# Kernel tuning notes

Measured on AMD Instinct MI355X. Metric: run time of the kernel, lower is better.

Reference implementation:

```python
import jax, jax.numpy as jnp
import numpy as np

USER_NUM = 80000
ITEM_NUM = 40000
N = USER_NUM + ITEM_NUM
EMB = 64
NNZ = 1200000
N_LAYERS = 3


def setup_inputs() -> dict:
    key = jax.random.key(0)
    k1, k2, k3, k4, k5 = jax.random.split(key, 5)
    # xavier_uniform bound for [num, emb]
    bu = float(np.sqrt(6.0 / (USER_NUM + EMB)))
    bi = float(np.sqrt(6.0 / (ITEM_NUM + EMB)))
    user_emb = jax.random.uniform(k1, (USER_NUM, EMB), jnp.float32, -bu, bu)
    item_emb = jax.random.uniform(k2, (ITEM_NUM, EMB), jnp.float32, -bi, bi)
    adj_rows = jax.random.randint(k3, (NNZ,), 0, N, dtype=jnp.int32)
    adj_cols = jax.random.randint(k4, (NNZ,), 0, N, dtype=jnp.int32)
    # normalized-adjacency-like positive values
    adj_vals = jax.random.uniform(k5, (NNZ,), jnp.float32) * (1.0 / 32.0)
    return {"user_emb": user_emb, "item_emb": item_emb,
            "adj_vals": adj_vals, "adj_rows": adj_rows, "adj_cols": adj_cols}


def _spmm(vals, rows, cols, x):
    # out[r] = sum_{e: rows[e]==r} vals[e] * x[cols[e]]   (COO SpMM)
    return jax.ops.segment_sum(vals[:, None] * x[cols], rows, num_segments=N)


def reference(user_emb, item_emb, adj_vals, adj_rows, adj_cols):
    ego = jnp.concatenate([user_emb, item_emb], axis=0)  # [N, d]
    acc = jnp.zeros_like(ego)
    for _ in range(N_LAYERS):
        ego = _spmm(adj_vals, adj_rows, adj_cols, ego)
        acc = acc + ego
    all_emb = acc / N_LAYERS  # mean over stacked layer outputs
    user_all = all_emb[:USER_NUM]
    item_all = all_emb[USER_NUM:]
    return (user_all, item_all)
```

## Files before the change

kernel.cpp:

```cpp
#include <hip/hip_runtime.h>
#include <hip/hip_fp16.h>

#define USER_NUM 80000
#define ITEM_NUM 40000
#define NNODE (USER_NUM + ITEM_NUM)
#define EMB 64
#define NB 469
#define P1_CHUNK 4096

#define HSCALE 8192.0f
#define HINV   (1.0f / 8192.0f)

__global__ void bucket_hist_kernel(const int* __restrict__ rows, int* __restrict__ bcounts, int nnz) {
    __shared__ int h[NB];
    for (int i = threadIdx.x; i < NB; i += blockDim.x) h[i] = 0;
    __syncthreads();
    int nq = nnz >> 2;
    int stride = gridDim.x * blockDim.x;
    for (int i = blockIdx.x * blockDim.x + threadIdx.x; i < nq; i += stride) {
        int4 r = ((const int4*)rows)[i];
        atomicAdd(&h[r.x >> 8], 1);
        atomicAdd(&h[r.y >> 8], 1);
        atomicAdd(&h[r.z >> 8], 1);
        atomicAdd(&h[r.w >> 8], 1);
    }
    if (blockIdx.x == 0) {
        for (int i = (nq << 2) + threadIdx.x; i < nnz; i += blockDim.x)
            atomicAdd(&h[rows[i] >> 8], 1);
    }
    __syncthreads();
    for (int i = threadIdx.x; i < NB; i += blockDim.x)
        if (h[i]) atomicAdd(&bcounts[i], h[i]);
}

__global__ void bucket_scan_kernel(const int* __restrict__ bcounts, int* __restrict__ bucket_off,
                                   int* __restrict__ bcursor, int* __restrict__ row_ptr, int nnz) {
    __shared__ int lds[512];
    int t = threadIdx.x;
    int v = (t < NB) ? bcounts[t] : 0;
    lds[t] = v;
    __syncthreads();
    for (int off = 1; off < 512; off <<= 1) {
        int add = (t >= off) ? lds[t - off] : 0;
        __syncthreads();
        lds[t] += add;
        __syncthreads();
    }
    if (t < NB) {
        int ex = lds[t] - v;
        bucket_off[t] = ex;
        bcursor[t]    = ex;
    }
    if (t == 0) { bucket_off[NB] = nnz; row_ptr[NNODE] = nnz; }
}

__global__ void phase1_kernel(const int* __restrict__ rows, const int* __restrict__ cols,
                              const float* __restrict__ vals, int* __restrict__ bcursor,
                              int2* __restrict__ tmp, int nnz) {
    __shared__ int h[NB];
    __shared__ int base[NB];
    int t = threadIdx.x;
    for (int i = t; i < NB; i += 256) h[i] = 0;
    __syncthreads();
    int lo = blockIdx.x * P1_CHUNK;
    int hi = lo + P1_CHUNK; if (hi > nnz) hi = nnz;
    int n4 = (hi - lo) >> 2;
    const int4*   rows4 = (const int4*)(rows + lo);
    const int4*   cols4 = (const int4*)(cols + lo);
    const float4* vals4 = (const float4*)(vals + lo);

    for (int i = t; i < n4; i += 256) {
        int4 r = rows4[i];
        atomicAdd(&h[r.x >> 8], 1);
        atomicAdd(&h[r.y >> 8], 1);
        atomicAdd(&h[r.z >> 8], 1);
        atomicAdd(&h[r.w >> 8], 1);
    }
    for (int i = lo + (n4 << 2) + t; i < hi; i += 256)
        atomicAdd(&h[rows[i] >> 8], 1);
    __syncthreads();
    for (int i = t; i < NB; i += 256) {
        int c = h[i];
        base[i] = c ? atomicAdd(&bcursor[i], c) : 0;
        h[i] = 0;
    }
    __syncthreads();
    for (int i = t; i < n4; i += 256) {
        int4 r = rows4[i];
        int4 c = cols4[i];
        float4 v = vals4[i];
        {
            int b = r.x >> 8; int loc = atomicAdd(&h[b], 1);
            tmp[base[b] + loc] = make_int2(c.x | ((r.x & 255) << 17), __float_as_int(v.x));
        }
        {
            int b = r.y >> 8; int loc = atomicAdd(&h[b], 1);
            tmp[base[b] + loc] = make_int2(c.y | ((r.y & 255) << 17), __float_as_int(v.y));
        }
        {
            int b = r.z >> 8; int loc = atomicAdd(&h[b], 1);
            tmp[base[b] + loc] = make_int2(c.z | ((r.z & 255) << 17), __float_as_int(v.z));
        }
        {
            int b = r.w >> 8; int loc = atomicAdd(&h[b], 1);
            tmp[base[b] + loc] = make_int2(c.w | ((r.w & 255) << 17), __float_as_int(v.w));
        }
    }
    for (int i = lo + (n4 << 2) + t; i < hi; i += 256) {
        int r = rows[i];
        int b = r >> 8;
        int loc = atomicAdd(&h[b], 1);
        tmp[base[b] + loc] = make_int2(cols[i] | ((r & 255) << 17), __float_as_int(vals[i]));
    }
}

__global__ void phase2_kernel(const int2* __restrict__ tmp, const int* __restrict__ bucket_off,
                              int* __restrict__ row_ptr, int2* __restrict__ edges) {
    __shared__ int hist[256];
    __shared__ int scan[256];
    __shared__ int cur[256];
    int b = blockIdx.x;
    int t = threadIdx.x;
    int row0  = b << 8;
    int nrows = NNODE - row0; if (nrows > 256) nrows = 256;
    int start = bucket_off[b];
    int end   = bucket_off[b + 1];
    hist[t] = 0;
    __syncthreads();
    for (int j = start + t; j < end; j += 256)
        atomicAdd(&hist[tmp[j].x >> 17], 1);
    __syncthreads();
    int v = hist[t];
    scan[t] = v;
    __syncthreads();
    for (int off = 1; off < 256; off <<= 1) {
        int add = (t >= off) ? scan[t - off] : 0;
        __syncthreads();
        scan[t] += add;
        __syncthreads();
    }
    int ex = scan[t] - v + start;
    if (t < nrows) row_ptr[row0 + t] = ex;
    cur[t] = ex;
    __syncthreads();
    for (int j = start + t; j < end; j += 256) {
        int2 e  = tmp[j];
        int rl  = e.x >> 17;
        int pos = atomicAdd(&cur[rl], 1);
        edges[pos] = make_int2(e.x & 0x1FFFF, e.y);
    }
}

__device__ __forceinline__ void load8(long long ev[8], const int2* __restrict__ edges,
                                      int sg, int eg, int j) {
    #pragma unroll
    for (int u = 0; u < 8; ++u) {
        int i = sg + j + u;
        ev[u] = (i < eg) ? *(const long long*)(edges + i) : 0LL;
    }
}

__device__ __forceinline__ float4 unpack_half4(uint2 gv) {
    float2 a = __half22float2(*(const __half2*)&gv.x);
    float2 b = __half22float2(*(const __half2*)&gv.y);
    return make_float4(a.x, a.y, b.x, b.y);
}

template <int LAYER>
__launch_bounds__(256)
__global__ void spmm_kernel(const float* __restrict__ xu, const float* __restrict__ xi,
                            const ushort* __restrict__ xh,
                            const int* __restrict__ row_ptr, const int2* __restrict__ edges,
                            ushort* __restrict__ yh, float* __restrict__ out) {
    int wave = (blockIdx.x * blockDim.x + threadIdx.x) >> 6;
    int lane = threadIdx.x & 63;
    int r0 = wave << 2;
    if (r0 >= NNODE) return;
    int g = lane >> 4;
    int c = lane & 15;

    int rp = 0;
    if (lane < 5) rp = row_ptr[r0 + lane];
    int p0 = __builtin_amdgcn_readlane(rp, 0);
    int p1 = __builtin_amdgcn_readlane(rp, 1);
    int p2 = __builtin_amdgcn_readlane(rp, 2);
    int p3 = __builtin_amdgcn_readlane(rp, 3);
    int p4 = __builtin_amdgcn_readlane(rp, 4);

    int sg = (g == 0) ? p0 : (g == 1) ? p1 : (g == 2) ? p2 : p3;
    int eg = (g == 0) ? p1 : (g == 1) ? p2 : (g == 2) ? p3 : p4;
    int maxd = max(max(p1 - p0, p2 - p1), max(p3 - p2, p4 - p3));

    float4 acc = make_float4(0.f, 0.f, 0.f, 0.f);

    if (maxd > 0) {
        long long ev[8];
        load8(ev, edges, sg, eg, 0);
        for (int j = 0; j < maxd; j += 8) {
            long long evn[8];
            if (j + 8 < maxd) load8(evn, edges, sg, eg, j + 8);
            #pragma unroll
            for (int u = 0; u < 8; ++u) {
                int   col = (int)(unsigned)ev[u];
                float v   = __int_as_float((int)(ev[u] >> 32));
                if (LAYER == 1) {
                    const float* q = (col < USER_NUM) ? xu + (size_t)col * EMB
                                                      : xi + (size_t)(col - USER_NUM) * EMB;
                    float4 gv = ((const float4*)q)[c];
                    acc.x += v * gv.x; acc.y += v * gv.y;
                    acc.z += v * gv.z; acc.w += v * gv.w;
                } else {
                    uint2 hv = ((const uint2*)(xh + (size_t)col * EMB))[c];
                    float4 gv = unpack_half4(hv);
                    acc.x += v * gv.x; acc.y += v * gv.y;
                    acc.z += v * gv.z; acc.w += v * gv.w;
                }
            }
            #pragma unroll
            for (int u = 0; u < 8; ++u) ev[u] = evn[u];
        }
    }

    int row = r0 + g;
    size_t oh = (size_t)row * EMB + (size_t)c * 4;

    if (LAYER == 1) {
        __half2 h0 = __floats2half2_rn(acc.x * HSCALE, acc.y * HSCALE);
        __half2 h1 = __floats2half2_rn(acc.z * HSCALE, acc.w * HSCALE);
        uint2 pk = make_uint2(*(const unsigned*)&h0, *(const unsigned*)&h1);
        *(uint2*)(yh + oh) = pk;
        *(float4*)(out + oh) = acc;
    } else if (LAYER == 2) {
        __half2 h0 = __floats2half2_rn(acc.x, acc.y);
        __half2 h1 = __floats2half2_rn(acc.z, acc.w);
        uint2 pk = make_uint2(*(const unsigned*)&h0, *(const unsigned*)&h1);
        *(uint2*)(yh + oh) = pk;
    } else {
        uint2 own = *(const uint2*)(xh + oh);
        float4 y2v = unpack_half4(own);
        float4 t = *(const float4*)(out + oh);
        const float s = 1.0f / 3.0f;
        t.x = (t.x + (y2v.x + acc.x) * HINV) * s;
        t.y = (t.y + (y2v.y + acc.y) * HINV) * s;
        t.z = (t.z + (y2v.z + acc.z) * HINV) * s;
        t.w = (t.w + (y2v.w + acc.w) * HINV) * s;
        *(float4*)(out + oh) = t;
    }
}

__global__ void init_kernel(const float* __restrict__ user_emb, const float* __restrict__ item_emb,
                            float* __restrict__ x, float* __restrict__ out) {
    int idx = blockIdx.x * blockDim.x + threadIdx.x;
    const int total = NNODE * EMB / 4;
    if (idx >= total) return;
    const int user_total = USER_NUM * EMB / 4;
    float4 v = (idx < user_total) ? ((const float4*)user_emb)[idx]
                                  : ((const float4*)item_emb)[idx - user_total];
    ((float4*)x)[idx]   = v;
    ((float4*)out)[idx] = make_float4(0.f, 0.f, 0.f, 0.f);
}

__global__ void scatter_kernel(const float* __restrict__ x, float* __restrict__ y,
                               const float* __restrict__ vals, const int* __restrict__ rows,
                               const int* __restrict__ cols, int nnz) {
    int tid = blockIdx.x * blockDim.x + threadIdx.x;
    int e = tid >> 4;
    if (e >= nnz) return;
    int c = tid & 15;
    int r = rows[e], col = cols[e];
    float v = vals[e];
    float4 xv = ((const float4*)(x + (size_t)col * EMB))[c];
    float* dst = y + (size_t)r * EMB + (size_t)c * 4;
    atomicAdd(dst + 0, xv.x * v);
    atomicAdd(dst + 1, xv.y * v);
    atomicAdd(dst + 2, xv.z * v);
    atomicAdd(dst + 3, xv.w * v);
}

__global__ void accum_kernel(float* __restrict__ out, const float* __restrict__ y, float scale) {
    int idx = blockIdx.x * blockDim.x + threadIdx.x;
    const int total = NNODE * EMB / 4;
    if (idx >= total) return;
    float4 o = ((float4*)out)[idx];
    float4 a = ((const float4*)y)[idx];
    o.x = (o.x + a.x) * scale; o.y = (o.y + a.y) * scale;
    o.z = (o.z + a.z) * scale; o.w = (o.w + a.w) * scale;
    ((float4*)out)[idx] = o;
}

extern "C" void kernel_launch(void* const* d_in, const int* in_sizes, int n_in,
                              void* d_out, int out_size, void* d_ws, size_t ws_size,
                              hipStream_t stream) {
    const float* user_emb = (const float*)d_in[0];
    const float* item_emb = (const float*)d_in[1];
    const float* vals     = (const float*)d_in[2];
    const int*   rows     = (const int*)d_in[3];
    const int*   cols     = (const int*)d_in[4];
    const int    nnz      = in_sizes[2];

    float* out = (float*)d_out;

    const size_t embN   = (size_t)NNODE * EMB;
    const size_t rp_pad = 120064;

    size_t need = (2 * embN + rp_pad) * 4 + (size_t)nnz * 8;

    if (ws_size >= need) {
        float* bufA    = (float*)d_ws;
        float* bufB    = bufA + embN;
        int*   row_ptr = (int*)(bufB + embN);
        int2*  edges   = (int2*)(row_ptr + rp_pad);

        int2* tmp        = (int2*)bufA;
        int*  bcounts    = (int*)bufB;
        int*  bucket_off = bcounts + 512;
        int*  bcursor    = bucket_off + 512;

        ushort* y1h = (ushort*)bufA;
        ushort* y2h = y1h + embN;

        hipMemsetAsync(bcounts, 0, NB * sizeof(int), stream);
        bucket_hist_kernel<<<256, 256, 0, stream>>>(rows, bcounts, nnz);
        bucket_scan_kernel<<<1, 512, 0, stream>>>(bcounts, bucket_off, bcursor, row_ptr, nnz);
        phase1_kernel<<<(nnz + P1_CHUNK - 1) / P1_CHUNK, 256, 0, stream>>>(rows, cols, vals, bcursor, tmp, nnz);
        phase2_kernel<<<NB, 256, 0, stream>>>(tmp, bucket_off, row_ptr, edges);

        const int nwaves = NNODE / 4;
        const int blocks = (nwaves * 64 + 255) / 256;
        spmm_kernel<1><<<blocks, 256, 0, stream>>>(user_emb, item_emb, nullptr, row_ptr, edges, y1h, out);
        spmm_kernel<2><<<blocks, 256, 0, stream>>>(nullptr, nullptr, y1h, row_ptr, edges, y2h, nullptr);
        spmm_kernel<3><<<blocks, 256, 0, stream>>>(nullptr, nullptr, y2h, row_ptr, edges, nullptr, out);
    } else {
        float* x = (float*)d_ws;
        float* y = x + embN;
        const size_t emb_bytes = embN * sizeof(float);
        {
            int total = NNODE * EMB / 4;
            init_kernel<<<(total + 255) / 256, 256, 0, stream>>>(user_emb, item_emb, x, out);
        }
        for (int layer = 0; layer < 3; ++layer) {
            hipMemsetAsync(y, 0, emb_bytes, stream);
            long long threads = (long long)nnz * 16;
            scatter_kernel<<<(int)((threads + 255) / 256), 256, 0, stream>>>(x, y, vals, rows, cols, nnz);
            int total = NNODE * EMB / 4;
            accum_kernel<<<(total + 255) / 256, 256, 0, stream>>>(out, y, layer < 2 ? 1.0f : (1.0f / 3.0f));
            float* t = x; x = y; y = t;
        }
    }
}
```

Measured before the change: 240.1 us.

## Drop fp32 layer-1 output write and widen edge batches to sixteen

Layer 1 no longer writes its fp32 result to the output buffer. Layer 3 instead rereads the scaled fp16 layer-1 copy, so the final mean is built from three terms in one step, removing one fp32 write and one fp32 read of the full embedding matrix. The edge loop now loads 16 edges per batch without software prefetch of the next batch, which means more gathers in flight per iteration but no overlap of edge loads with compute. The layer-1 term now comes from its fp16 copy, which adds rounding error compared with the fp32 value.

```diff
diff --git a/kernel.cpp b/kernel.cpp
--- a/kernel.cpp
+++ b/kernel.cpp
@@ -151,10 +151,10 @@
     }
 }
 
-__device__ __forceinline__ void load8(long long ev[8], const int2* __restrict__ edges,
-                                      int sg, int eg, int j) {
+__device__ __forceinline__ void load16(long long ev[16], const int2* __restrict__ edges,
+                                       int sg, int eg, int j) {
     #pragma unroll
-    for (int u = 0; u < 8; ++u) {
+    for (int u = 0; u < 16; ++u) {
         int i = sg + j + u;
         ev[u] = (i < eg) ? *(const long long*)(edges + i) : 0LL;
     }
@@ -171,7 +171,8 @@
 __global__ void spmm_kernel(const float* __restrict__ xu, const float* __restrict__ xi,
                             const ushort* __restrict__ xh,
                             const int* __restrict__ row_ptr, const int2* __restrict__ edges,
-                            ushort* __restrict__ yh, float* __restrict__ out) {
+                            ushort* __restrict__ yh,
+                            const ushort* __restrict__ y1h_own, float* __restrict__ out) {
     int wave = (blockIdx.x * blockDim.x + threadIdx.x) >> 6;
     int lane = threadIdx.x & 63;
     int r0 = wave << 2;
@@ -193,31 +194,25 @@
 
     float4 acc = make_float4(0.f, 0.f, 0.f, 0.f);
 
-    if (maxd > 0) {
-        long long ev[8];
-        load8(ev, edges, sg, eg, 0);
-        for (int j = 0; j < maxd; j += 8) {
-            long long evn[8];
-            if (j + 8 < maxd) load8(evn, edges, sg, eg, j + 8);
-            #pragma unroll
-            for (int u = 0; u < 8; ++u) {
-                int   col = (int)(unsigned)ev[u];
-                float v   = __int_as_float((int)(ev[u] >> 32));
-                if (LAYER == 1) {
-                    const float* q = (col < USER_NUM) ? xu + (size_t)col * EMB
-                                                      : xi + (size_t)(col - USER_NUM) * EMB;
-                    float4 gv = ((const float4*)q)[c];
-                    acc.x += v * gv.x; acc.y += v * gv.y;
-                    acc.z += v * gv.z; acc.w += v * gv.w;
-                } else {
-                    uint2 hv = ((const uint2*)(xh + (size_t)col * EMB))[c];
-                    float4 gv = unpack_half4(hv);
-                    acc.x += v * gv.x; acc.y += v * gv.y;
-                    acc.z += v * gv.z; acc.w += v * gv.w;
-                }
+    for (int j = 0; j < maxd; j += 16) {
+        long long ev[16];
+        load16(ev, edges, sg, eg, j);
+        #pragma unroll
+        for (int u = 0; u < 16; ++u) {
+            int   col = (int)(unsigned)ev[u];
+            float v   = __int_as_float((int)(ev[u] >> 32));
+            if (LAYER == 1) {
+                const float* q = (col < USER_NUM) ? xu + (size_t)col * EMB
+                                                  : xi + (size_t)(col - USER_NUM) * EMB;
+                float4 gv = ((const float4*)q)[c];
+                acc.x += v * gv.x; acc.y += v * gv.y;
+                acc.z += v * gv.z; acc.w += v * gv.w;
+            } else {
+                uint2 hv = ((const uint2*)(xh + (size_t)col * EMB))[c];
+                float4 gv = unpack_half4(hv);
+                acc.x += v * gv.x; acc.y += v * gv.y;
+                acc.z += v * gv.z; acc.w += v * gv.w;
             }
-            #pragma unroll
-            for (int u = 0; u < 8; ++u) ev[u] = evn[u];
         }
     }
 
@@ -229,21 +224,22 @@
         __half2 h1 = __floats2half2_rn(acc.z * HSCALE, acc.w * HSCALE);
         uint2 pk = make_uint2(*(const unsigned*)&h0, *(const unsigned*)&h1);
         *(uint2*)(yh + oh) = pk;
-        *(float4*)(out + oh) = acc;
     } else if (LAYER == 2) {
         __half2 h0 = __floats2half2_rn(acc.x, acc.y);
         __half2 h1 = __floats2half2_rn(acc.z, acc.w);
         uint2 pk = make_uint2(*(const unsigned*)&h0, *(const unsigned*)&h1);
         *(uint2*)(yh + oh) = pk;
     } else {
-        uint2 own = *(const uint2*)(xh + oh);
-        float4 y2v = unpack_half4(own);
-        float4 t = *(const float4*)(out + oh);
-        const float s = 1.0f / 3.0f;
-        t.x = (t.x + (y2v.x + acc.x) * HINV) * s;
-        t.y = (t.y + (y2v.y + acc.y) * HINV) * s;
-        t.z = (t.z + (y2v.z + acc.z) * HINV) * s;
-        t.w = (t.w + (y2v.w + acc.w) * HINV) * s;
+        uint2 o1 = *(const uint2*)(y1h_own + oh);
+        uint2 o2 = *(const uint2*)(xh + oh);
+        float4 y1v = unpack_half4(o1);
+        float4 y2v = unpack_half4(o2);
+        const float s = HINV / 3.0f;
+        float4 t;
+        t.x = (y1v.x + y2v.x + acc.x) * s;
+        t.y = (y1v.y + y2v.y + acc.y) * s;
+        t.z = (y1v.z + y2v.z + acc.z) * s;
+        t.w = (y1v.w + y2v.w + acc.w) * s;
         *(float4*)(out + oh) = t;
     }
 }
@@ -327,9 +323,9 @@
 
         const int nwaves = NNODE / 4;
         const int blocks = (nwaves * 64 + 255) / 256;
-        spmm_kernel<1><<<blocks, 256, 0, stream>>>(user_emb, item_emb, nullptr, row_ptr, edges, y1h, out);
-        spmm_kernel<2><<<blocks, 256, 0, stream>>>(nullptr, nullptr, y1h, row_ptr, edges, y2h, nullptr);
-        spmm_kernel<3><<<blocks, 256, 0, stream>>>(nullptr, nullptr, y2h, row_ptr, edges, nullptr, out);
+        spmm_kernel<1><<<blocks, 256, 0, stream>>>(user_emb, item_emb, nullptr, row_ptr, edges, y1h, nullptr, nullptr);
+        spmm_kernel<2><<<blocks, 256, 0, stream>>>(nullptr, nullptr, y1h, row_ptr, edges, y2h, nullptr, nullptr);
+        spmm_kernel<3><<<blocks, 256, 0, stream>>>(nullptr, nullptr, y2h, row_ptr, edges, nullptr, y1h, out);
     } else {
         float* x = (float*)d_ws;
         float* y = x + embN;
```

Result: no change. 235.9 us (-1.7%).
